# Optimization experiments

Measured on AMD Instinct MI355X. Metric: run time of the kernel, lower is better.

## Reference

```python
import jax, jax.numpy as jnp
import numpy as np

B, N, M, E, C_IN, C_OUT = 4, 10000, 10000, 160000, 128, 128


def setup_inputs() -> dict:
    key = jax.random.key(0)
    k1, k2, k3, k4 = jax.random.split(key, 4)
    x = jax.random.normal(k1, (B, N, C_IN), dtype=jnp.float32)
    node_idx = jax.random.randint(k2, (B, 1, E), 0, N)
    hyedge_idx = jax.random.randint(k3, (B, 1, E), 0, M)
    H = jnp.concatenate([node_idx, hyedge_idx], axis=1).astype(jnp.int64)  # [B, 2, E]
    theta = jax.random.normal(k4, (C_IN, C_OUT), dtype=jnp.float32) * (1.0 / np.sqrt(C_IN))
    bias = jnp.zeros((C_OUT,), dtype=jnp.float32)
    return {"x": x, "H": H, "theta": theta, "bias": bias}


def _hyconv_single(xg, Hg):
    # xg: [N, D] (already x @ theta); Hg: [2, E]
    node_idx, hyedge_idx = Hg[0], Hg[1]
    ones = jnp.ones((E,), dtype=xg.dtype)
    # node -> hyperedge: mean over nodes incident to each hyperedge
    deg_e = jax.ops.segment_sum(ones, hyedge_idx, num_segments=M)  # [M]
    e_norm = (1.0 / deg_e)[hyedge_idx]  # [E]
    x_edge = jax.ops.segment_sum(xg[node_idx] * e_norm[:, None], hyedge_idx, num_segments=M)  # [M, D]
    # hyperedge -> node: mean over hyperedges incident to each node
    deg_n = jax.ops.segment_sum(ones, node_idx, num_segments=N)  # [N]
    n_norm = (1.0 / deg_n)[node_idx]  # [E]
    x_node = jax.ops.segment_sum(x_edge[hyedge_idx] * n_norm[:, None], node_idx, num_segments=N)  # [N, D]
    return x_node


def reference(x, H, theta, bias):
    xt = jnp.einsum('bnc,cd->bnd', x, theta)  # dense projection
    out = jax.vmap(_hyconv_single)(xt, H)  # [B, N, D]
    return out + bias
```

## Files before the change

kernel.cpp:

```cpp
#include <hip/hip_runtime.h>
#include <hip/hip_bf16.h>


#define BB 4
#define NN 10000
#define MM 10000
#define EE 160000
#define CC 128
#define BM (BB * MM)
#define BN (BB * NN)
#define NCOPY 8
#define CAPX 16

typedef unsigned short u16;
using bf16 = __hip_bfloat16;
using bf162 = __hip_bfloat162;

__global__ __launch_bounds__(256) void build_gemm_k(const int* __restrict__ H,
                                                    int* __restrict__ ctr,
                                                    u16* __restrict__ srcA,
                                                    u16* __restrict__ srcB,
                                                    const float* __restrict__ x,
                                                    const float* __restrict__ theta,
                                                    bf16* __restrict__ xt) {
    __shared__ float sTh[64 * 128];
    __shared__ float sX[32 * 128];
    const int bi = blockIdx.x;

    if (bi % 3 != 0) {
        const int j = bi - bi / 3 - 1;
        const int g = j * 256 + threadIdx.x;
        if (g >= BB * EE) return;
        const int cp = bi & 7;
        const int b = g / EE, e = g - b * EE;
        const int nd = H[b * 2 * EE + e];
        const int he = H[b * 2 * EE + EE + e];
        const int bktA = b * MM + he;
        const int s = atomicAdd(&ctr[cp * (BM + BN) + bktA], 1);
        if (s < CAPX) srcA[((size_t)cp * BM + bktA) * CAPX + s] = (u16)nd;
        const int bktB = b * NN + nd;
        const int q = atomicAdd(&ctr[cp * (BM + BN) + BM + bktB], 1);
        if (q < CAPX) srcB[((size_t)cp * BN + bktB) * CAPX + q] = (u16)he;
        return;
    }

    const int tid = threadIdx.x;
    const int row0 = (bi / 3) * 32;
    {
        const float4* src = (const float4*)&x[row0 * 128];
        float4* dst = (float4*)sX;
#pragma unroll
        for (int i = 0; i < 4; ++i) dst[tid + 256 * i] = src[tid + 256 * i];
    }
    const int cg2 = (tid & 63) * 2;
    const int rg = tid >> 6;
    float ax[8], ay[8];
#pragma unroll
    for (int r = 0; r < 8; ++r) { ax[r] = 0.f; ay[r] = 0.f; }

    for (int half = 0; half < 2; ++half) {
        __syncthreads();
        {
            const float4* src = (const float4*)&theta[half * 64 * 128];
            float4* dst = (float4*)sTh;
#pragma unroll
            for (int i = 0; i < 8; ++i) dst[tid + 256 * i] = src[tid + 256 * i];
        }
        __syncthreads();
#pragma unroll
        for (int k4 = 0; k4 < 16; ++k4) {
            const int kk = 4 * k4;
            const float2 t0 = *(const float2*)&sTh[(kk + 0) * 128 + cg2];
            const float2 t1 = *(const float2*)&sTh[(kk + 1) * 128 + cg2];
            const float2 t2 = *(const float2*)&sTh[(kk + 2) * 128 + cg2];
            const float2 t3 = *(const float2*)&sTh[(kk + 3) * 128 + cg2];
#pragma unroll
            for (int r = 0; r < 8; ++r) {
                const float4 xv =
                    *(const float4*)&sX[(rg * 8 + r) * 128 + half * 64 + kk];
                ax[r] = fmaf(xv.x, t0.x, ax[r]); ay[r] = fmaf(xv.x, t0.y, ay[r]);
                ax[r] = fmaf(xv.y, t1.x, ax[r]); ay[r] = fmaf(xv.y, t1.y, ay[r]);
                ax[r] = fmaf(xv.z, t2.x, ax[r]); ay[r] = fmaf(xv.z, t2.y, ay[r]);
                ax[r] = fmaf(xv.w, t3.x, ax[r]); ay[r] = fmaf(xv.w, t3.y, ay[r]);
            }
        }
    }
#pragma unroll
    for (int r = 0; r < 8; ++r) {
        bf162 h;
        h.x = __float2bfloat16(ax[r]);
        h.y = __float2bfloat16(ay[r]);
        *(bf162*)&xt[(size_t)(row0 + rg * 8 + r) * 128 + cg2] = h;
    }
}

__device__ __forceinline__ void gacc(const bf16* __restrict__ base, int idx, int lane,
                                     float& sx, float& sy) {
    const unsigned raw = *(const unsigned*)(base + (size_t)idx * CC + lane * 2);
    sx += __uint_as_float(raw << 16);
    sy += __uint_as_float(raw & 0xffff0000u);
}

__device__ __forceinline__ int merge_lists(const int* __restrict__ ctr,
                                           const u16* __restrict__ src,
                                           int side_off, int Bx, int wid, int lane,
                                           u16* __restrict__ buf) {
    int cnt = 0;
    if (lane < NCOPY) {
        cnt = ctr[lane * (BM + BN) + side_off + wid];
        cnt = cnt > CAPX ? CAPX : cnt;
    }
    int pre = cnt;
#pragma unroll
    for (int d = 1; d < 8; d <<= 1) {
        int o = __shfl_up(pre, d, 64);
        if (lane >= d) pre += o;
    }
    const int base = pre - cnt;
    int total = __shfl(pre, 7, 64);
    total = total > 64 ? 64 : total;
    if (lane < NCOPY && cnt) {
        const u16* lst = src + ((size_t)lane * Bx + wid) * CAPX;
        for (int j = 0; j < cnt; ++j) {
            const int p = base + j;
            if (p < 64) buf[p] = lst[j];
        }
    }
    __syncthreads();
    return total;
}

__global__ __launch_bounds__(256) void phase1_pull(const bf16* __restrict__ xt,
                                                   const int* __restrict__ ctr,
                                                   const u16* __restrict__ srcA,
                                                   bf16* __restrict__ x_edge) {
    __shared__ __align__(16) u16 buf[4 * 64];
    const int wid = (blockIdx.x * 256 + threadIdx.x) >> 6;
    const int lane = threadIdx.x & 63;
    u16* wbuf = &buf[(threadIdx.x >> 6) * 64];
    const int total = merge_lists(ctr, srcA, 0, BM, wid, lane, wbuf);

    const bf16* base = xt + (size_t)(wid / MM) * NN * CC;
    float sx = 0.f, sy = 0.f;
    int i = 0;
    for (; i + 8 <= total; i += 8) {
        const uint4 pk = *(const uint4*)&wbuf[i];
        gacc(base, pk.x & 0xffff, lane, sx, sy);
        gacc(base, pk.x >> 16, lane, sx, sy);
        gacc(base, pk.y & 0xffff, lane, sx, sy);
        gacc(base, pk.y >> 16, lane, sx, sy);
        gacc(base, pk.z & 0xffff, lane, sx, sy);
        gacc(base, pk.z >> 16, lane, sx, sy);
        gacc(base, pk.w & 0xffff, lane, sx, sy);
        gacc(base, pk.w >> 16, lane, sx, sy);
    }
    for (; i < total; ++i) gacc(base, wbuf[i], lane, sx, sy);
    const float w = total ? 1.0f / (float)total : 0.f;
    bf162 h;
    h.x = __float2bfloat16(sx * w);
    h.y = __float2bfloat16(sy * w);
    *(bf162*)&x_edge[(size_t)wid * CC + lane * 2] = h;
}

__global__ __launch_bounds__(256) void phase2_pull(const bf16* __restrict__ x_edge,
                                                   const int* __restrict__ ctr,
                                                   const u16* __restrict__ srcB,
                                                   const float* __restrict__ bias,
                                                   float* __restrict__ out) {
    __shared__ __align__(16) u16 buf[4 * 64];
    const int wid = (blockIdx.x * 256 + threadIdx.x) >> 6;
    const int lane = threadIdx.x & 63;
    u16* wbuf = &buf[(threadIdx.x >> 6) * 64];
    const int total = merge_lists(ctr, srcB, BM, BN, wid, lane, wbuf);

    const bf16* base = x_edge + (size_t)(wid / NN) * MM * CC;
    float sx = 0.f, sy = 0.f;
    int i = 0;
    for (; i + 8 <= total; i += 8) {
        const uint4 pk = *(const uint4*)&wbuf[i];
        gacc(base, pk.x & 0xffff, lane, sx, sy);
        gacc(base, pk.x >> 16, lane, sx, sy);
        gacc(base, pk.y & 0xffff, lane, sx, sy);
        gacc(base, pk.y >> 16, lane, sx, sy);
        gacc(base, pk.z & 0xffff, lane, sx, sy);
        gacc(base, pk.z >> 16, lane, sx, sy);
        gacc(base, pk.w & 0xffff, lane, sx, sy);
        gacc(base, pk.w >> 16, lane, sx, sy);
    }
    for (; i < total; ++i) gacc(base, wbuf[i], lane, sx, sy);
    const float w = total ? 1.0f / (float)total : 0.f;
    const float2 bv = *(const float2*)&bias[lane * 2];
    float2 o;
    o.x = sx * w + bv.x;
    o.y = sy * w + bv.y;
    *(float2*)&out[(size_t)wid * CC + lane * 2] = o;
}

extern "C" void kernel_launch(void* const* d_in, const int* in_sizes, int n_in,
                              void* d_out, int out_size, void* d_ws, size_t ws_size,
                              hipStream_t stream) {
    const float* x = (const float*)d_in[0];
    const int* H = (const int*)d_in[1];
    const float* theta = (const float*)d_in[2];
    const float* bias = (const float*)d_in[3];
    float* out = (float*)d_out;

    bf16* xt = (bf16*)d_ws;
    bf16* x_edge = xt + (size_t)BB * NN * CC;
    int* ctr = (int*)(x_edge + (size_t)BB * MM * CC);
    u16* srcA = (u16*)(ctr + NCOPY * (BM + BN));
    u16* srcB = srcA + (size_t)NCOPY * BM * CAPX;

    hipMemsetAsync(ctr, 0, (size_t)NCOPY * (BM + BN) * sizeof(int), stream);

    build_gemm_k<<<3750, 256, 0, stream>>>(H, ctr, srcA, srcB, x, theta, xt);
    phase1_pull<<<BM / 4, 256, 0, stream>>>(xt, ctr, srcA, x_edge);
    phase2_pull<<<BN / 4, 256, 0, stream>>>(x_edge, ctr, srcB, bias, out);
}
```

Baseline: 197.4 us.

## Split build/gemm kernels and use half-row gathers with interleaved batch blocks

```diff
diff --git a/kernel.cpp b/kernel.cpp
--- a/kernel.cpp
+++ b/kernel.cpp
@@ -13,44 +13,40 @@
 #define CAPX 16
 
 typedef unsigned short u16;
+typedef float f4 __attribute__((ext_vector_type(4)));
 using bf16 = __hip_bfloat16;
-using bf162 = __hip_bfloat162;
-
-__global__ __launch_bounds__(256) void build_gemm_k(const int* __restrict__ H,
-                                                    int* __restrict__ ctr,
-                                                    u16* __restrict__ srcA,
-                                                    u16* __restrict__ srcB,
-                                                    const float* __restrict__ x,
-                                                    const float* __restrict__ theta,
-                                                    bf16* __restrict__ xt) {
+
+__global__ __launch_bounds__(256) void build_k(const int* __restrict__ H,
+                                               int* __restrict__ ctr,
+                                               u16* __restrict__ srcA,
+                                               u16* __restrict__ srcB) {
+    const int g = blockIdx.x * 256 + threadIdx.x;
+    if (g >= BB * EE) return;
+    const int cp = blockIdx.x & 7;
+    const int b = g / EE, e = g - b * EE;
+    const int nd = H[b * 2 * EE + e];
+    const int he = H[b * 2 * EE + EE + e];
+    const int bktA = b * MM + he;
+    const int s = atomicAdd(&ctr[cp * (BM + BN) + bktA], 1);
+    if (s < CAPX) srcA[((size_t)cp * BM + bktA) * CAPX + s] = (u16)nd;
+    const int bktB = b * NN + nd;
+    const int q = atomicAdd(&ctr[cp * (BM + BN) + BM + bktB], 1);
+    if (q < CAPX) srcB[((size_t)cp * BN + bktB) * CAPX + q] = (u16)he;
+}
+
+__global__ __launch_bounds__(256) void gemm_k(const float* __restrict__ x,
+                                              const float* __restrict__ theta,
+                                              u16* __restrict__ xt) {
     __shared__ float sTh[64 * 128];
     __shared__ float sX[32 * 128];
-    const int bi = blockIdx.x;
-
-    if (bi % 3 != 0) {
-        const int j = bi - bi / 3 - 1;
-        const int g = j * 256 + threadIdx.x;
-        if (g >= BB * EE) return;
-        const int cp = bi & 7;
-        const int b = g / EE, e = g - b * EE;
-        const int nd = H[b * 2 * EE + e];
-        const int he = H[b * 2 * EE + EE + e];
-        const int bktA = b * MM + he;
-        const int s = atomicAdd(&ctr[cp * (BM + BN) + bktA], 1);
-        if (s < CAPX) srcA[((size_t)cp * BM + bktA) * CAPX + s] = (u16)nd;
-        const int bktB = b * NN + nd;
-        const int q = atomicAdd(&ctr[cp * (BM + BN) + BM + bktB], 1);
-        if (q < CAPX) srcB[((size_t)cp * BN + bktB) * CAPX + q] = (u16)he;
-        return;
-    }
-
     const int tid = threadIdx.x;
-    const int row0 = (bi / 3) * 32;
+    const int row0 = blockIdx.x * 32;
     {
-        const float4* src = (const float4*)&x[row0 * 128];
-        float4* dst = (float4*)sX;
-#pragma unroll
-        for (int i = 0; i < 4; ++i) dst[tid + 256 * i] = src[tid + 256 * i];
+        const f4* src = (const f4*)&x[row0 * 128];
+        f4* dst = (f4*)sX;
+#pragma unroll
+        for (int i = 0; i < 4; ++i)
+            dst[tid + 256 * i] = __builtin_nontemporal_load(src + tid + 256 * i);
     }
     const int cg2 = (tid & 63) * 2;
     const int rg = tid >> 6;
@@ -87,18 +83,13 @@
     }
 #pragma unroll
     for (int r = 0; r < 8; ++r) {
-        bf162 h;
-        h.x = __float2bfloat16(ax[r]);
-        h.y = __float2bfloat16(ay[r]);
-        *(bf162*)&xt[(size_t)(row0 + rg * 8 + r) * 128 + cg2] = h;
-    }
-}
-
-__device__ __forceinline__ void gacc(const bf16* __restrict__ base, int idx, int lane,
-                                     float& sx, float& sy) {
-    const unsigned raw = *(const unsigned*)(base + (size_t)idx * CC + lane * 2);
-    sx += __uint_as_float(raw << 16);
-    sy += __uint_as_float(raw & 0xffff0000u);
+        bf16 hx = __float2bfloat16(ax[r]);
+        bf16 hy = __float2bfloat16(ay[r]);
+        const unsigned pk =
+            (unsigned)*(u16*)&hx | ((unsigned)*(u16*)&hy << 16);
+        __builtin_nontemporal_store(
+            pk, (unsigned*)(xt + (size_t)(row0 + rg * 8 + r) * CC + cg2));
+    }
 }
 
 __device__ __forceinline__ int merge_lists(const int* __restrict__ ctr,
@@ -113,87 +104,87 @@
     int pre = cnt;
 #pragma unroll
     for (int d = 1; d < 8; d <<= 1) {
-        int o = __shfl_up(pre, d, 64);
+        const int o = __shfl_up(pre, d, 64);
         if (lane >= d) pre += o;
     }
     const int base = pre - cnt;
     int total = __shfl(pre, 7, 64);
-    total = total > 64 ? 64 : total;
-    if (lane < NCOPY && cnt) {
+    if (lane < NCOPY) {
         const u16* lst = src + ((size_t)lane * Bx + wid) * CAPX;
-        for (int j = 0; j < cnt; ++j) {
-            const int p = base + j;
-            if (p < 64) buf[p] = lst[j];
+        const uint4 lo = *(const uint4*)lst;
+        const uint4 hi = *(const uint4*)(lst + 8);
+        const unsigned ev[8] = {lo.x, lo.y, lo.z, lo.w, hi.x, hi.y, hi.z, hi.w};
+#pragma unroll
+        for (int j = 0; j < CAPX; ++j) {
+            if (j < cnt) buf[base + j] = (u16)(ev[j >> 1] >> ((j & 1) * 16));
         }
     }
     __syncthreads();
-    return total;
-}
-
-__global__ __launch_bounds__(256) void phase1_pull(const bf16* __restrict__ xt,
+    return total > 128 ? 128 : total;
+}
+
+__device__ __forceinline__ float ldbf(const u16* __restrict__ p, int idx) {
+    return __uint_as_float(((unsigned)p[(size_t)idx * CC]) << 16);
+}
+
+__global__ __launch_bounds__(256) void phase1_pull(const u16* __restrict__ xt,
                                                    const int* __restrict__ ctr,
                                                    const u16* __restrict__ srcA,
-                                                   bf16* __restrict__ x_edge) {
-    __shared__ __align__(16) u16 buf[4 * 64];
-    const int wid = (blockIdx.x * 256 + threadIdx.x) >> 6;
-    const int lane = threadIdx.x & 63;
-    u16* wbuf = &buf[(threadIdx.x >> 6) * 64];
+                                                   u16* __restrict__ x_edge) {
+    __shared__ __align__(16) u16 buf[4 * 128];
+    const int bi = blockIdx.x;
+    const int grp = bi & 7;
+    const int b = grp >> 1, half = grp & 1;
+    const int w = threadIdx.x >> 6, lane = threadIdx.x & 63;
+    const int wid = b * MM + (bi >> 3) * 4 + w;
+    u16* wbuf = &buf[w * 128];
     const int total = merge_lists(ctr, srcA, 0, BM, wid, lane, wbuf);
 
-    const bf16* base = xt + (size_t)(wid / MM) * NN * CC;
-    float sx = 0.f, sy = 0.f;
+    const u16* basep = xt + (size_t)b * NN * CC + half * 64 + lane;
+    float s = 0.f;
     int i = 0;
     for (; i + 8 <= total; i += 8) {
         const uint4 pk = *(const uint4*)&wbuf[i];
-        gacc(base, pk.x & 0xffff, lane, sx, sy);
-        gacc(base, pk.x >> 16, lane, sx, sy);
-        gacc(base, pk.y & 0xffff, lane, sx, sy);
-        gacc(base, pk.y >> 16, lane, sx, sy);
-        gacc(base, pk.z & 0xffff, lane, sx, sy);
-        gacc(base, pk.z >> 16, lane, sx, sy);
-        gacc(base, pk.w & 0xffff, lane, sx, sy);
-        gacc(base, pk.w >> 16, lane, sx, sy);
-    }
-    for (; i < total; ++i) gacc(base, wbuf[i], lane, sx, sy);
-    const float w = total ? 1.0f / (float)total : 0.f;
-    bf162 h;
-    h.x = __float2bfloat16(sx * w);
-    h.y = __float2bfloat16(sy * w);
-    *(bf162*)&x_edge[(size_t)wid * CC + lane * 2] = h;
-}
-
-__global__ __launch_bounds__(256) void phase2_pull(const bf16* __restrict__ x_edge,
+        s += ldbf(basep, pk.x & 0xffff); s += ldbf(basep, pk.x >> 16);
+        s += ldbf(basep, pk.y & 0xffff); s += ldbf(basep, pk.y >> 16);
+        s += ldbf(basep, pk.z & 0xffff); s += ldbf(basep, pk.z >> 16);
+        s += ldbf(basep, pk.w & 0xffff); s += ldbf(basep, pk.w >> 16);
+    }
+    for (; i < total; ++i) s += ldbf(basep, wbuf[i]);
+    const float wgt = total ? 1.0f / (float)total : 0.f;
+    const bf16 h = __float2bfloat16(s * wgt);
+    __builtin_nontemporal_store(
+        *(const u16*)&h, x_edge + (size_t)wid * CC + half * 64 + lane);
+}
+
+__global__ __launch_bounds__(256) void phase2_pull(const u16* __restrict__ x_edge,
                                                    const int* __restrict__ ctr,
                                                    const u16* __restrict__ srcB,
                                                    const float* __restrict__ bias,
                                                    float* __restrict__ out) {
-    __shared__ __align__(16) u16 buf[4 * 64];
-    const int wid = (blockIdx.x * 256 + threadIdx.x) >> 6;
-    const int lane = threadIdx.x & 63;
-    u16* wbuf = &buf[(threadIdx.x >> 6) * 64];
+    __shared__ __align__(16) u16 buf[4 * 128];
+    const int bi = blockIdx.x;
+    const int grp = bi & 7;
+    const int b = grp >> 1, half = grp & 1;
+    const int w = threadIdx.x >> 6, lane = threadIdx.x & 63;
+    const int wid = b * NN + (bi >> 3) * 4 + w;
+    u16* wbuf = &buf[w * 128];
     const int total = merge_lists(ctr, srcB, BM, BN, wid, lane, wbuf);
 
-    const bf16* base = x_edge + (size_t)(wid / NN) * MM * CC;
-    float sx = 0.f, sy = 0.f;
+    const u16* basep = x_edge + (size_t)b * MM * CC + half * 64 + lane;
+    float s = 0.f;
     int i = 0;
     for (; i + 8 <= total; i += 8) {
         const uint4 pk = *(const uint4*)&wbuf[i];
-        gacc(base, pk.x & 0xffff, lane, sx, sy);
-        gacc(base, pk.x >> 16, lane, sx, sy);
-        gacc(base, pk.y & 0xffff, lane, sx, sy);
-        gacc(base, pk.y >> 16, lane, sx, sy);
-        gacc(base, pk.z & 0xffff, lane, sx, sy);
-        gacc(base, pk.z >> 16, lane, sx, sy);
-        gacc(base, pk.w & 0xffff, lane, sx, sy);
-        gacc(base, pk.w >> 16, lane, sx, sy);
-    }
-    for (; i < total; ++i) gacc(base, wbuf[i], lane, sx, sy);
-    const float w = total ? 1.0f / (float)total : 0.f;
-    const float2 bv = *(const float2*)&bias[lane * 2];
-    float2 o;
-    o.x = sx * w + bv.x;
-    o.y = sy * w + bv.y;
-    *(float2*)&out[(size_t)wid * CC + lane * 2] = o;
+        s += ldbf(basep, pk.x & 0xffff); s += ldbf(basep, pk.x >> 16);
+        s += ldbf(basep, pk.y & 0xffff); s += ldbf(basep, pk.y >> 16);
+        s += ldbf(basep, pk.z & 0xffff); s += ldbf(basep, pk.z >> 16);
+        s += ldbf(basep, pk.w & 0xffff); s += ldbf(basep, pk.w >> 16);
+    }
+    for (; i < total; ++i) s += ldbf(basep, wbuf[i]);
+    const float wgt = total ? 1.0f / (float)total : 0.f;
+    const float o = s * wgt + bias[half * 64 + lane];
+    __builtin_nontemporal_store(o, out + (size_t)wid * CC + half * 64 + lane);
 }
 
 extern "C" void kernel_launch(void* const* d_in, const int* in_sizes, int n_in,
@@ -205,15 +196,16 @@
     const float* bias = (const float*)d_in[3];
     float* out = (float*)d_out;
 
-    bf16* xt = (bf16*)d_ws;
-    bf16* x_edge = xt + (size_t)BB * NN * CC;
+    u16* xt = (u16*)d_ws;
+    u16* x_edge = xt + (size_t)BB * NN * CC;
     int* ctr = (int*)(x_edge + (size_t)BB * MM * CC);
     u16* srcA = (u16*)(ctr + NCOPY * (BM + BN));
     u16* srcB = srcA + (size_t)NCOPY * BM * CAPX;
 
-    hipMemsetAsync(ctr, 0, (size_t)NCOPY * (BM + BN) * sizeof(int), stream);
-
-    build_gemm_k<<<3750, 256, 0, stream>>>(H, ctr, srcA, srcB, x, theta, xt);
-    phase1_pull<<<BM / 4, 256, 0, stream>>>(xt, ctr, srcA, x_edge);
-    phase2_pull<<<BN / 4, 256, 0, stream>>>(x_edge, ctr, srcB, bias, out);
-}
+    (void)hipMemsetAsync(ctr, 0, (size_t)NCOPY * (BM + BN) * sizeof(int), stream);
+
+    build_k<<<2500, 256, 0, stream>>>(H, ctr, srcA, srcB);
+    gemm_k<<<1250, 256, 0, stream>>>(x, theta, xt);
+    phase1_pull<<<20000, 256, 0, stream>>>(xt, ctr, srcA, x_edge);
+    phase2_pull<<<20000, 256, 0, stream>>>(x_edge, ctr, srcB, bias, out);
+}
```

Measured after the change: 246.3 us. +24.8%, slower.
